# Kernel optimization log

Hardware: AMD Instinct MI355X
Metric: run time of the kernel (lower is better)

The kernel has to match this reference:

```python
import jax, jax.numpy as jnp
import numpy as np

K1, K2, K3 = 6, 4, 3  # knn_graph k (loop=True -> self included, dist 0 is always top)


def _sqdist(a, b):
    # a: [B,N,3], b: [B,M,3] -> [B,N,M] squared euclidean distances
    an = jnp.sum(a * a, -1)[:, :, None]
    bn = jnp.sum(b * b, -1)[:, None, :]
    return an + bn - 2.0 * jnp.einsum('bnd,bmd->bnm', a, b)


def _knn_idx(pos, k):
    # for each point, indices of its k nearest neighbors (self included, loop=True)
    d = _sqdist(pos, pos)                 # [B,N,N]
    _, idx = jax.lax.top_k(-d, k)         # [B,N,k]
    return idx


def _gather(a, idx):
    # a: [B,N,...], idx: [B,...] -> per-cloud gather
    return jax.vmap(lambda ab, ib: ab[ib])(a, idx)


def _fps(pos, m):
    # farthest point sampling on one cloud [N,3], deterministic start at index 0
    min_d = jnp.sum((pos - pos[0]) ** 2, -1)  # [N]

    def step(min_d, _):
        idx = jnp.argmax(min_d)
        d = jnp.sum((pos - pos[idx]) ** 2, -1)
        return jnp.minimum(min_d, d), idx

    _, idxs = jax.lax.scan(step, min_d, None, length=m - 1)
    return jnp.concatenate([jnp.zeros((1,), dtype=idxs.dtype), idxs])


def _pn_layer(h, pos, k, W1, b1, W2, b2):
    # PointNetLayer: gather h_i/h_j/pos_i/pos_j over knn edges, MLP, max-aggregate
    idx = _knn_idx(pos, k)                       # [B,N,k]
    h_j = _gather(h, idx)                        # [B,N,k,C]
    pos_j = _gather(pos, idx)                    # [B,N,k,3]
    rel = pos_j - pos[:, :, None, :]             # pos_j - pos_i
    h_i = jnp.broadcast_to(h[:, :, None, :], h_j.shape)
    inp = jnp.concatenate([h_i, h_j, rel], -1)   # [B,N,k,2C+3]
    msg = jnp.maximum(inp @ W1 + b1, 0.0) @ W2 + b2
    return jnp.max(msg, axis=2)                  # scatter-max == dense max over k


def _forward(x, pos, W11, b11, W12, b12, W21, b21, W22, b22, W31, b31, W32, b32, Wr, br):
    h = jax.nn.relu(_pn_layer(x, pos, K1, W11, b11, W12, b12))
    idx = jax.vmap(lambda p: _fps(p, p.shape[0] // 2))(pos)   # ratio=0.5
    pos, h = _gather(pos, idx), _gather(h, idx)
    h = jax.nn.relu(_pn_layer(h, pos, K2, W21, b21, W22, b22))
    idx = jax.vmap(lambda p: _fps(p, p.shape[0] // 2))(pos)
    pos, h = _gather(pos, idx), _gather(h, idx)
    h = jax.nn.relu(_pn_layer(h, pos, K3, W31, b31, W32, b32))
    g = jnp.max(h, axis=1)                        # global_max_pool
    return g @ Wr + br                            # [B,10]


def _lin(key, fin, fout):
    k1, k2 = jax.random.split(key)
    lim = 1.0 / np.sqrt(fin)
    W = jax.random.uniform(k1, (fin, fout), minval=-lim, maxval=lim, dtype=jnp.float32)
    b = jax.random.uniform(k2, (fout,), minval=-lim, maxval=lim, dtype=jnp.float32)
    return W, b


def setup_inputs() -> dict:
    key = jax.random.key(0)
    ks = jax.random.split(key, 10)
    B, N = 16, 4096
    x = jax.random.normal(ks[0], (B, N, 1), dtype=jnp.float32)
    pos = jax.random.uniform(ks[1], (B, N, 3), dtype=jnp.float32)
    W11, b11 = _lin(ks[2], 1 * 2 + 3, 32)
    W12, b12 = _lin(ks[3], 32, 32)
    W21, b21 = _lin(ks[4], 32 * 2 + 3, 32)
    W22, b22 = _lin(ks[5], 32, 32)
    W31, b31 = _lin(ks[6], 32 * 2 + 3, 32)
    W32, b32 = _lin(ks[7], 32, 32)
    Wr, br = _lin(ks[8], 32, 10)
    return dict(x=x, pos=pos, W11=W11, b11=b11, W12=W12, b12=b12,
                W21=W21, b21=b21, W22=W22, b22=b22,
                W31=W31, b31=b31, W32=W32, b32=b32, Wr=Wr, br=br)


def reference(x, pos, W11, b11, W12, b12, W21, b21, W22, b22, W31, b31, W32, b32, Wr, br):
    return _forward(x, pos, W11, b11, W12, b12, W21, b21, W22, b22,
                    W31, b31, W32, b32, Wr, br)
```

## Files before the change

kernel.cpp:

```cpp
#include <hip/hip_runtime.h>

#define BATCH 16
#define NP1 4096
#define NP2 2048
#define NP3 1024

typedef float v2f __attribute__((ext_vector_type(2)));

__device__ __forceinline__ float f_add(float a, float b) { return __fadd_rn(a, b); }
__device__ __forceinline__ float f_mul(float a, float b) { return __fmul_rn(a, b); }
__device__ __forceinline__ float f_sub(float a, float b) { return __fsub_rn(a, b); }
__device__ __forceinline__ float sqnorm3(float x, float y, float z) {
  return f_add(f_add(f_mul(x, x), f_mul(y, y)), f_mul(z, z));
}

__device__ __forceinline__ unsigned long long u64max(unsigned long long a,
                                                     unsigned long long b) {
  return a > b ? a : b;
}
__device__ __forceinline__ unsigned long long u64min(unsigned long long a,
                                                     unsigned long long b) {
  return a < b ? a : b;
}
__device__ __forceinline__ double dmax(double a, double b) { return __builtin_fmax(a, b); }

template<int CTRL, int RMASK>
__device__ __forceinline__ unsigned long long dpp_u64(unsigned long long k) {
  const int lo = __builtin_amdgcn_update_dpp(0, (int)(unsigned)k, CTRL, RMASK, 0xF, true);
  const int hi = __builtin_amdgcn_update_dpp(0, (int)(unsigned)(k >> 32), CTRL, RMASK, 0xF, true);
  return ((unsigned long long)(unsigned)hi << 32) | (unsigned)lo;
}
template<int CTRL, int RMASK>
__device__ __forceinline__ double dpp_dbl(double v) {
  return __longlong_as_double(
      (long long)dpp_u64<CTRL, RMASK>((unsigned long long)__double_as_longlong(v)));
}

#define KBIAS 0x00100000u

__device__ __forceinline__ double wave_max_keyd(double k) {
  k = dmax(k, dpp_dbl<0x111, 0xF>(k));
  k = dmax(k, dpp_dbl<0x112, 0xF>(k));
  k = dmax(k, dpp_dbl<0x114, 0xF>(k));
  k = dmax(k, dpp_dbl<0x118, 0xF>(k));
  k = dmax(k, dpp_dbl<0x142, 0xA>(k));
  k = dmax(k, dpp_dbl<0x143, 0xC>(k));
  return k;
}

template<int N, int M>
__device__ void fps_block(char* __restrict__ smem, const float* __restrict__ P,
                          int* __restrict__ samp, float* __restrict__ pos_out)
{
#pragma clang fp contract(off)
  constexpr int THREADS = 512;
  constexpr int E = N / THREADS;
  constexpr int P2 = E / 2;
  float4* pos4 = (float4*)smem;
  unsigned short* ord = (unsigned short*)(smem + 16 * N);
  int* sampL = (int*)(smem + 18 * N);
  unsigned* cursor = (unsigned*)(smem + 18 * N + 4 * M);
  double* kslots = (double*)(smem + 18 * N + 4 * M + 32);
  const int tid = threadIdx.x;
  const int lane = tid & 63, wv = tid >> 6;
  if (tid < 8) cursor[tid] = 0u;
  __syncthreads();
  int oct[E];
#pragma unroll
  for (int e = 0; e < E; ++e) {
    const int t = e * THREADS + tid;
    const float x = P[t * 3], y = P[t * 3 + 1], z = P[t * 3 + 2];
    pos4[t] = make_float4(x, y, z, 0.f);
    oct[e] = (x > 0.5f ? 1 : 0) | (y > 0.5f ? 2 : 0) | (z > 0.5f ? 4 : 0);
    atomicAdd(&cursor[oct[e]], 1u);
  }
  __syncthreads();
  if (tid == 0) {
    unsigned run = 0;
#pragma unroll
    for (int o = 0; o < 8; ++o) { const unsigned c = cursor[o]; cursor[o] = run; run += c; }
  }
  __syncthreads();
#pragma unroll
  for (int e = 0; e < E; ++e) {
    const unsigned d = atomicAdd(&cursor[oct[e]], 1u);
    ord[d] = (unsigned short)(e * THREADS + tid);
  }
  __syncthreads();
  const float4 p0 = pos4[0];
  const float x0 = p0.x, y0 = p0.y, z0 = p0.z;
  v2f X2[P2], Y2[P2], Z2[P2], MD2[P2];
  unsigned ILO[E];
  double key = 0.0;
  float mnx = 1e30f, mny = 1e30f, mnz = 1e30f;
  float mxx = -1e30f, mxy = -1e30f, mxz = -1e30f;
  {
    const v2f x0v = {x0, x0}, y0v = {y0, y0}, z0v = {z0, z0};
#pragma unroll
    for (int p = 0; p < P2; ++p) {
      const int q0 = wv * (64 * E) + (2 * p) * 64 + lane;
      const int o0 = ord[q0], o1 = ord[q0 + 64];
      const float4 a0 = pos4[o0], a1 = pos4[o1];
      X2[p] = (v2f){a0.x, a1.x}; Y2[p] = (v2f){a0.y, a1.y}; Z2[p] = (v2f){a0.z, a1.z};
      mnx = fminf(mnx, fminf(a0.x, a1.x)); mxx = fmaxf(mxx, fmaxf(a0.x, a1.x));
      mny = fminf(mny, fminf(a0.y, a1.y)); mxy = fmaxf(mxy, fmaxf(a0.y, a1.y));
      mnz = fminf(mnz, fminf(a0.z, a1.z)); mxz = fmaxf(mxz, fmaxf(a0.z, a1.z));
      const v2f dx = X2[p] - x0v, dy = Y2[p] - y0v, dz = Z2[p] - z0v;
      MD2[p] = (dx * dx + dy * dy) + dz * dz;
      ILO[2 * p]     = 0xFFFFFFFFu - (unsigned)o0;
      ILO[2 * p + 1] = 0xFFFFFFFFu - (unsigned)o1;
      const unsigned long long k0 =
          ((unsigned long long)(__float_as_uint(MD2[p].x) + KBIAS) << 32) | ILO[2 * p];
      const unsigned long long k1 =
          ((unsigned long long)(__float_as_uint(MD2[p].y) + KBIAS) << 32) | ILO[2 * p + 1];
      key = dmax(key, dmax(__longlong_as_double((long long)k0),
                           __longlong_as_double((long long)k1)));
    }
  }
#pragma unroll
  for (int off = 1; off < 64; off <<= 1) {
    mnx = fminf(mnx, __shfl_xor(mnx, off)); mxx = fmaxf(mxx, __shfl_xor(mxx, off));
    mny = fminf(mny, __shfl_xor(mny, off)); mxy = fmaxf(mxy, __shfl_xor(mxy, off));
    mnz = fminf(mnz, __shfl_xor(mnz, off)); mxz = fmaxf(mxz, __shfl_xor(mxz, off));
  }
  if (tid == 0) sampL[0] = 0;
  bool dirty = true;
  double wkey = 0.0;
#pragma unroll 1
  for (int s = 1; s < M; ++s) {
    if (dirty) wkey = wave_max_keyd(key);
    const int pb = s & 1;
    if (lane == 63) kslots[pb * 8 + wv] = wkey;
    __syncthreads();
    double v0 = kslots[pb * 8 + 0], v1 = kslots[pb * 8 + 1];
    double v2 = kslots[pb * 8 + 2], v3 = kslots[pb * 8 + 3];
    double v4 = kslots[pb * 8 + 4], v5 = kslots[pb * 8 + 5];
    double v6 = kslots[pb * 8 + 6], v7 = kslots[pb * 8 + 7];
    v0 = dmax(v0, v1); v2 = dmax(v2, v3); v4 = dmax(v4, v5); v6 = dmax(v6, v7);
    v0 = dmax(v0, v2); v4 = dmax(v4, v6);
    v0 = dmax(v0, v4);
    const unsigned long long kb = (unsigned long long)__double_as_longlong(v0);
    const int gi = (int)(0xFFFFFFFFu - (unsigned)kb);
    const float4 sp = pos4[gi];
    if (tid == 0) sampL[s] = gi;
    const float mdx = fmaxf(fmaxf(f_sub(mnx, sp.x), f_sub(sp.x, mxx)), 0.f);
    const float mdy = fmaxf(fmaxf(f_sub(mny, sp.y), f_sub(sp.y, mxy)), 0.f);
    const float mdz = fmaxf(fmaxf(f_sub(mnz, sp.z), f_sub(sp.z, mxz)), 0.f);
    const float mind2 = sqnorm3(mdx, mdy, mdz);
    const unsigned wmhi = (unsigned)__builtin_amdgcn_readlane(
        (int)(unsigned)((unsigned long long)__double_as_longlong(wkey) >> 32), 63) - KBIAS;
    const float wmaxf = __uint_as_float(wmhi);
    if (mind2 < wmaxf) {
      dirty = true;
      key = 0.0;
      const v2f sxv = {sp.x, sp.x}, syv = {sp.y, sp.y}, szv = {sp.z, sp.z};
#pragma unroll
      for (int p = 0; p < P2; ++p) {
        const v2f dx = X2[p] - sxv, dy = Y2[p] - syv, dz = Z2[p] - szv;
        const v2f d = (dx * dx + dy * dy) + dz * dz;
        MD2[p] = __builtin_elementwise_min(MD2[p], d);
        const unsigned long long k0 =
            ((unsigned long long)(__float_as_uint(MD2[p].x) + KBIAS) << 32) | ILO[2 * p];
        const unsigned long long k1 =
            ((unsigned long long)(__float_as_uint(MD2[p].y) + KBIAS) << 32) | ILO[2 * p + 1];
        key = dmax(key, dmax(__longlong_as_double((long long)k0),
                             __longlong_as_double((long long)k1)));
      }
    } else {
      dirty = false;
    }
  }
  __syncthreads();
  for (int s2 = tid; s2 < M; s2 += THREADS) {
    const int g = sampL[s2];
    samp[s2] = g;
    const float4 sp2 = pos4[g];
    pos_out[3 * s2 + 0] = sp2.x;
    pos_out[3 * s2 + 1] = sp2.y;
    pos_out[3 * s2 + 2] = sp2.z;
  }
}

__device__ __forceinline__ float f4c(const float4& v, int c) {
  return c == 0 ? v.x : c == 1 ? v.y : c == 2 ? v.z : v.w;
}
__device__ __forceinline__ void fma4(float4& a, float v, const float4& w) {
  a.x += v * w.x; a.y += v * w.y; a.z += v * w.z; a.w += v * w.w;
}

template<int K, int C>
__device__ void pn_compute(
    const float4* __restrict__ sW1, const float4* __restrict__ sW2,
    const float* __restrict__ sb1, const float* __restrict__ sb2,
    const float* __restrict__ P, const float* __restrict__ Hsrc,
    const int* __restrict__ hmap, int i, float xi, float yi, float zi,
    const int* kn, float* __restrict__ outrow)
{
  float4 abase[8];
#pragma unroll
  for (int o = 0; o < 8; ++o)
    abase[o] = make_float4(sb1[4 * o], sb1[4 * o + 1], sb1[4 * o + 2], sb1[4 * o + 3]);
  if constexpr (C == 1) {
    const float v = Hsrc[hmap ? hmap[i] : i];
#pragma unroll
    for (int o = 0; o < 8; ++o) fma4(abase[o], v, sW1[o]);
  } else {
    const int ri = hmap ? hmap[i] : i;
    const float4* Hi = (const float4*)(Hsrc + (size_t)ri * C);
#pragma unroll
    for (int c4 = 0; c4 < C / 4; ++c4) {
      const float4 hv = Hi[c4];
#pragma unroll
      for (int q = 0; q < 4; ++q) {
        const float v = f4c(hv, q);
#pragma unroll
        for (int o = 0; o < 8; ++o) fma4(abase[o], v, sW1[(4 * c4 + q) * 8 + o]);
      }
    }
  }
  float4 best[8];
#pragma unroll
  for (int o = 0; o < 8; ++o)
    best[o] = make_float4(-__builtin_inff(), -__builtin_inff(), -__builtin_inff(), -__builtin_inff());

  auto edge_pair = [&](int j0, int j1) {
    float4 a0[8], a1[8];
#pragma unroll
    for (int o = 0; o < 8; ++o) { a0[o] = abase[o]; a1[o] = abase[o]; }
    const float rx0 = P[j0 * 3] - xi, ry0 = P[j0 * 3 + 1] - yi, rz0 = P[j0 * 3 + 2] - zi;
    const float rx1 = P[j1 * 3] - xi, ry1 = P[j1 * 3 + 1] - yi, rz1 = P[j1 * 3 + 2] - zi;
    if constexpr (C == 1) {
      const float v0 = Hsrc[hmap ? hmap[j0] : j0], v1 = Hsrc[hmap ? hmap[j1] : j1];
#pragma unroll
      for (int o = 0; o < 8; ++o) {
        const float4 w = sW1[C * 8 + o];
        fma4(a0[o], v0, w); fma4(a1[o], v1, w);
      }
    } else {
      const int r0i = hmap ? hmap[j0] : j0, r1i = hmap ? hmap[j1] : j1;
      const float4* Hj0 = (const float4*)(Hsrc + (size_t)r0i * C);
      const float4* Hj1 = (const float4*)(Hsrc + (size_t)r1i * C);
#pragma unroll
      for (int c4 = 0; c4 < C / 4; ++c4) {
        const float4 h0 = Hj0[c4], h1 = Hj1[c4];
#pragma unroll
        for (int q = 0; q < 4; ++q) {
          const float v0 = f4c(h0, q), v1 = f4c(h1, q);
#pragma unroll
          for (int o = 0; o < 8; ++o) {
            const float4 w = sW1[(C + 4 * c4 + q) * 8 + o];
            fma4(a0[o], v0, w); fma4(a1[o], v1, w);
          }
        }
      }
    }
    const float r0[3] = {rx0, ry0, rz0}, r1[3] = {rx1, ry1, rz1};
#pragma unroll
    for (int r = 0; r < 3; ++r) {
#pragma unroll
      for (int o = 0; o < 8; ++o) {
        const float4 w = sW1[(2 * C + r) * 8 + o];
        fma4(a0[o], r0[r], w); fma4(a1[o], r1[r], w);
      }
    }
#pragma unroll
    for (int o = 0; o < 8; ++o) {
      a0[o].x = fmaxf(a0[o].x, 0.f); a0[o].y = fmaxf(a0[o].y, 0.f);
      a0[o].z = fmaxf(a0[o].z, 0.f); a0[o].w = fmaxf(a0[o].w, 0.f);
      a1[o].x = fmaxf(a1[o].x, 0.f); a1[o].y = fmaxf(a1[o].y, 0.f);
      a1[o].z = fmaxf(a1[o].z, 0.f); a1[o].w = fmaxf(a1[o].w, 0.f);
    }
#pragma unroll
    for (int hf = 0; hf < 2; ++hf) {
      float4 m0[4], m1[4];
#pragma unroll
      for (int o4 = 0; o4 < 4; ++o4) {
        const int c0 = 16 * hf + 4 * o4;
        m0[o4] = make_float4(sb2[c0], sb2[c0 + 1], sb2[c0 + 2], sb2[c0 + 3]);
        m1[o4] = m0[o4];
      }
#pragma unroll
      for (int c = 0; c < 32; ++c) {
        const float v0 = f4c(a0[c >> 2], c & 3), v1 = f4c(a1[c >> 2], c & 3);
#pragma unroll
        for (int o4 = 0; o4 < 4; ++o4) {
          const float4 w = sW2[c * 8 + hf * 4 + o4];
          fma4(m0[o4], v0, w); fma4(m1[o4], v1, w);
        }
      }
#pragma unroll
      for (int o4 = 0; o4 < 4; ++o4) {
        float4& bb = best[hf * 4 + o4];
        bb.x = fmaxf(bb.x, fmaxf(m0[o4].x, m1[o4].x));
        bb.y = fmaxf(bb.y, fmaxf(m0[o4].y, m1[o4].y));
        bb.z = fmaxf(bb.z, fmaxf(m0[o4].z, m1[o4].z));
        bb.w = fmaxf(bb.w, fmaxf(m0[o4].w, m1[o4].w));
      }
    }
  };

#pragma unroll
  for (int e = 0; e + 1 < K; e += 2) edge_pair(kn[e], kn[e + 1]);

  float4* ho = (float4*)outrow;
#pragma unroll
  for (int o = 0; o < 8; ++o)
    ho[o] = make_float4(fmaxf(best[o].x, 0.0f), fmaxf(best[o].y, 0.0f),
                        fmaxf(best[o].z, 0.0f), fmaxf(best[o].w, 0.0f));
}

template<int K, int NC, int C, int THREADS>
__device__ void fused_knn_pn(char* __restrict__ smem,
    const float* __restrict__ P, const float* __restrict__ Hsrc,
    const int* __restrict__ hmap,
    const float* __restrict__ W1, const float* __restrict__ b1,
    const float* __restrict__ W2, const float* __restrict__ b2,
    float* __restrict__ hout, int s)
{
  constexpr int CIN = 2 * C + 3;
  float4* tile = (float4*)smem;
  float4* sW1 = (float4*)(smem + 16 * 1024);
  float4* sW2 = sW1 + CIN * 8;
  float* sb1 = (float*)(sW2 + 32 * 8);
  float* sb2 = sb1 + 32;
  const int tid = threadIdx.x;
  for (int t = tid; t < CIN * 8; t += THREADS) sW1[t] = ((const float4*)W1)[t];
  for (int t = tid; t < 32 * 8; t += THREADS) sW2[t] = ((const float4*)W2)[t];
  if (tid < 32) { sb1[tid] = b1[tid]; sb2[tid] = b2[tid]; }

  const float xi = P[s * 3], yi = P[s * 3 + 1], zi = P[s * 3 + 2];
  const float ni = sqnorm3(xi, yi, zi);
  float bd[K]; int bj[K];
#pragma unroll
  for (int t = 0; t < K; ++t) { bd[t] = __builtin_inff(); bj[t] = 0; }
  for (int base = 0; base < NC; base += 1024) {
    __syncthreads();
    for (int t = tid; t < 1024; t += THREADS) {
      const float* q = P + (size_t)(base + t) * 3;
      const float x = q[0], y = q[1], z = q[2];
      tile[t] = make_float4(x, y, z, sqnorm3(x, y, z));
    }
    __syncthreads();
#pragma unroll 2
    for (int t = 0; t < 1024; ++t) {
      const float4 q = tile[t];
      const float dot = f_add(f_add(f_mul(xi, q.x), f_mul(yi, q.y)), f_mul(zi, q.z));
      const float d = f_sub(f_add(ni, q.w), f_mul(2.0f, dot));
      if (d < bd[K - 1]) {
        bd[K - 1] = d; bj[K - 1] = base + t;
#pragma unroll
        for (int r = K - 1; r > 0; --r) {
          if (bd[r] < bd[r - 1]) {
            float td = bd[r]; bd[r] = bd[r - 1]; bd[r - 1] = td;
            int   tj = bj[r]; bj[r] = bj[r - 1]; bj[r - 1] = tj;
          } else break;
        }
      }
    }
  }
  pn_compute<K, C>(sW1, sW2, sb1, sb2, P, Hsrc, hmap, s, xi, yi, zi, bj,
                   hout + (size_t)s * 32);
}

template<int K, int NC>
__device__ void fused_knn_pn_quad(char* __restrict__ smem,
    const float* __restrict__ P, const float* __restrict__ Hsrc,
    const int* __restrict__ hmap,
    const float* __restrict__ W1, const float* __restrict__ b1,
    const float* __restrict__ W2, const float* __restrict__ b2,
    float* __restrict__ hout, int s, int q)
{
  constexpr int THREADS = 256;
  constexpr int RQ = NC / 4;
  constexpr int CIN = 67;
  float4* tile = (float4*)smem;
  float4* sW1 = (float4*)(smem + 16 * (NC + 4));
  float4* sW2 = sW1 + CIN * 8;
  float* sb1 = (float*)(sW2 + 32 * 8);
  float* sb2 = sb1 + 32;
  const int tid = threadIdx.x;

  for (int t = tid; t < NC; t += THREADS) {
    const float* c = P + (size_t)t * 3;
    const float x = c[0], y = c[1], z = c[2];
    tile[t + t / RQ] = make_float4(x, y, z, sqnorm3(x, y, z));
  }
  for (int t = tid; t < CIN * 8; t += THREADS) sW1[t] = ((const float4*)W1)[t];
  for (int t = tid; t < 32 * 8; t += THREADS) sW2[t] = ((const float4*)W2)[t];
  if (tid < 32) { sb1[tid] = b1[tid]; sb2[tid] = b2[tid]; }
  __syncthreads();

  const float4 qv = tile[s + s / RQ];
  const float xi = qv.x, yi = qv.y, zi = qv.z, ni = qv.w;
  float bd[4]; int bj[4];
#pragma unroll
  for (int t = 0; t < 4; ++t) { bd[t] = __builtin_inff(); bj[t] = 0; }
  const int sbase = q * (RQ + 1);
#pragma unroll 2
  for (int t = 0; t < RQ; ++t) {
    const float4 c = tile[sbase + t];
    const float dot = f_add(f_add(f_mul(xi, c.x), f_mul(yi, c.y)), f_mul(zi, c.z));
    const float d = f_sub(f_add(ni, c.w), f_mul(2.0f, dot));
    if (d < bd[3]) {
      bd[3] = d; bj[3] = q * RQ + t;
#pragma unroll
      for (int r = 3; r > 0; --r) {
        if (bd[r] < bd[r - 1]) {
          float td = bd[r]; bd[r] = bd[r - 1]; bd[r - 1] = td;
          int   tj = bj[r]; bj[r] = bj[r - 1]; bj[r - 1] = tj;
        } else break;
      }
    }
  }
  unsigned long long a0, a1, a2, a3;
  {
    auto mk = [](float d, int j) {
      unsigned u = __float_as_uint(d);
      u ^= (unsigned)((int)u >> 31) | 0x80000000u;
      return ((unsigned long long)u << 32) | (unsigned)j;
    };
    a0 = mk(bd[0], bj[0]); a1 = mk(bd[1], bj[1]);
    a2 = mk(bd[2], bj[2]); a3 = mk(bd[3], bj[3]);
  }
  {
    const unsigned long long b0 = __shfl_xor(a0, 1), b1_ = __shfl_xor(a1, 1),
                             b2_ = __shfl_xor(a2, 1), b3_ = __shfl_xor(a3, 1);
    const unsigned long long t0 = u64min(a0, b3_), t1 = u64min(a1, b2_),
                             t2 = u64min(a2, b1_), t3 = u64min(a3, b0);
    const unsigned long long u0 = u64min(t0, t2), u2 = u64max(t0, t2),
                             u1 = u64min(t1, t3), u3 = u64max(t1, t3);
    a0 = u64min(u0, u1); a1 = u64max(u0, u1);
    a2 = u64min(u2, u3); a3 = u64max(u2, u3);
  }
  {
    const unsigned long long b0 = __shfl_xor(a0, 2), b1_ = __shfl_xor(a1, 2),
                             b2_ = __shfl_xor(a2, 2), b3_ = __shfl_xor(a3, 2);
    const unsigned long long t0 = u64min(a0, b3_), t1 = u64min(a1, b2_),
                             t2 = u64min(a2, b1_), t3 = u64min(a3, b0);
    const unsigned long long u0 = u64min(t0, t2), u2 = u64max(t0, t2),
                             u1 = u64min(t1, t3), u3 = u64max(t1, t3);
    a0 = u64min(u0, u1); a1 = u64max(u0, u1);
    a2 = u64min(u2, u3); a3 = u64max(u2, u3);
  }
  const int e = (q < K) ? q : (K - 1);
  const unsigned long long ke = (e == 0) ? a0 : (e == 1) ? a1 : (e == 2) ? a2 : a3;
  const int jn = (int)(unsigned)ke;

  const int ri = hmap ? hmap[s] : s;
  const int rj = hmap ? hmap[jn] : jn;
  float4 acc[8];
#pragma unroll
  for (int o = 0; o < 8; ++o)
    acc[o] = make_float4(sb1[4 * o], sb1[4 * o + 1], sb1[4 * o + 2], sb1[4 * o + 3]);
  const float4* Hi = (const float4*)(Hsrc + (size_t)ri * 32);
#pragma unroll
  for (int c4 = 0; c4 < 8; ++c4) {
    const float4 hv = Hi[c4];
#pragma unroll
    for (int t = 0; t < 4; ++t) {
      const float v = f4c(hv, t);
#pragma unroll
      for (int o = 0; o < 8; ++o) fma4(acc[o], v, sW1[(4 * c4 + t) * 8 + o]);
    }
  }
  const float4* Hj = (const float4*)(Hsrc + (size_t)rj * 32);
#pragma unroll
  for (int c4 = 0; c4 < 8; ++c4) {
    const float4 hv = Hj[c4];
#pragma unroll
    for (int t = 0; t < 4; ++t) {
      const float v = f4c(hv, t);
#pragma unroll
      for (int o = 0; o < 8; ++o) fma4(acc[o], v, sW1[(32 + 4 * c4 + t) * 8 + o]);
    }
  }
  const float4 cj = tile[jn + jn / RQ];
  const float r3[3] = {cj.x - xi, cj.y - yi, cj.z - zi};
#pragma unroll
  for (int r = 0; r < 3; ++r)
#pragma unroll
    for (int o = 0; o < 8; ++o) fma4(acc[o], r3[r], sW1[(64 + r) * 8 + o]);
#pragma unroll
  for (int o = 0; o < 8; ++o) {
    acc[o].x = fmaxf(acc[o].x, 0.f); acc[o].y = fmaxf(acc[o].y, 0.f);
    acc[o].z = fmaxf(acc[o].z, 0.f); acc[o].w = fmaxf(acc[o].w, 0.f);
  }
  float4 m[8];
#pragma unroll
  for (int o = 0; o < 8; ++o)
    m[o] = make_float4(sb2[4 * o], sb2[4 * o + 1], sb2[4 * o + 2], sb2[4 * o + 3]);
#pragma unroll
  for (int c = 0; c < 32; ++c) {
    const float v = f4c(acc[c >> 2], c & 3);
#pragma unroll
    for (int o = 0; o < 8; ++o) fma4(m[o], v, sW2[c * 8 + o]);
  }
#pragma unroll
  for (int o = 0; o < 8; ++o) {
    float4 v = m[o];
    v.x = fmaxf(v.x, __shfl_xor(v.x, 1)); v.y = fmaxf(v.y, __shfl_xor(v.y, 1));
    v.z = fmaxf(v.z, __shfl_xor(v.z, 1)); v.w = fmaxf(v.w, __shfl_xor(v.w, 1));
    v.x = fmaxf(v.x, __shfl_xor(v.x, 2)); v.y = fmaxf(v.y, __shfl_xor(v.y, 2));
    v.z = fmaxf(v.z, __shfl_xor(v.z, 2)); v.w = fmaxf(v.w, __shfl_xor(v.w, 2));
    m[o] = v;
  }
  float4* ho = (float4*)(hout + (size_t)s * 32);
  {
    const float4 v0 = m[2 * q], v1 = m[2 * q + 1];
    ho[2 * q] = make_float4(fmaxf(v0.x, 0.f), fmaxf(v0.y, 0.f),
                            fmaxf(v0.z, 0.f), fmaxf(v0.w, 0.f));
    ho[2 * q + 1] = make_float4(fmaxf(v1.x, 0.f), fmaxf(v1.y, 0.f),
                                fmaxf(v1.z, 0.f), fmaxf(v1.w, 0.f));
  }
}

__global__ __launch_bounds__(512) void megaA(
    const float* __restrict__ x, const float* __restrict__ pos,
    const float* __restrict__ W11, const float* __restrict__ b11,
    const float* __restrict__ W12, const float* __restrict__ b12,
    int* __restrict__ samp1, float* __restrict__ pos2, float* __restrict__ h1full)
{
  __shared__ __align__(16) char smem[82112];
  if (blockIdx.x < BATCH) {
    const int b = blockIdx.x;
    fps_block<NP1, NP2>(smem, pos + (size_t)b * NP1 * 3, samp1 + b * NP2,
                        pos2 + (size_t)b * NP2 * 3);
  } else {
    const int id = blockIdx.x - BATCH;
    const int b = id >> 3;
    const int s = (id & 7) * 512 + threadIdx.x;
    fused_knn_pn<6, NP1, 1, 512>(smem, pos + (size_t)b * NP1 * 3, x + (size_t)b * NP1,
                                 nullptr, W11, b11, W12, b12,
                                 h1full + (size_t)b * NP1 * 32, s);
  }
}

__global__ __launch_bounds__(256) void megaB(
    const float* __restrict__ pos2, const int* __restrict__ samp1,
    const float* __restrict__ h1full,
    const float* __restrict__ W21, const float* __restrict__ b21,
    const float* __restrict__ W22, const float* __restrict__ b22,
    float* __restrict__ h2out)
{
  __shared__ __align__(16) char smem[(2048 + 4) * 16 + 67 * 8 * 16 + 32 * 8 * 16 + 256];
  const int b = blockIdx.x >> 4;
  const int s = ((blockIdx.x & 15) << 6) + (threadIdx.x >> 2);
  const int q = threadIdx.x & 3;
  fused_knn_pn_quad<4, NP2>(smem, pos2 + (size_t)b * NP2 * 3,
                            h1full + (size_t)b * NP1 * 32, samp1 + b * NP2,
                            W21, b21, W22, b22, h2out + (size_t)b * NP3 * 32, s, q);
}

__global__ __launch_bounds__(256) void megaC(
    const float* __restrict__ pos2, const float* __restrict__ h2out,
    const float* __restrict__ W31, const float* __restrict__ b31,
    const float* __restrict__ W32, const float* __restrict__ b32,
    float* __restrict__ h3full)
{
  __shared__ __align__(16) char smem[(1024 + 4) * 16 + 67 * 8 * 16 + 32 * 8 * 16 + 256];
  const int b = blockIdx.x >> 4;
  const int s = ((blockIdx.x & 15) << 6) + (threadIdx.x >> 2);
  const int q = threadIdx.x & 3;
  fused_knn_pn_quad<3, NP3>(smem, pos2 + (size_t)b * NP2 * 3,
                            h2out + (size_t)b * NP3 * 32, nullptr,
                            W31, b31, W32, b32, h3full + (size_t)b * NP3 * 32, s, q);
}

__global__ __launch_bounds__(256) void final_kernel(
    const float* __restrict__ h, const float* __restrict__ Wr,
    const float* __restrict__ br, float* __restrict__ out)
{
  __shared__ float red[8][32];
  __shared__ float g[32];
  const int b = blockIdx.x;
  const int c = threadIdx.x & 31, grp = threadIdx.x >> 5;
  const float* H = h + (size_t)b * NP3 * 32;
  float m = -__builtin_inff();
  for (int r = grp; r < NP3; r += 8) m = fmaxf(m, H[r * 32 + c]);
  red[grp][c] = m;
  __syncthreads();
  if (threadIdx.x < 32) {
    float v = red[0][c];
#pragma unroll
    for (int w = 1; w < 8; ++w) v = fmaxf(v, red[w][c]);
    g[c] = v;
  }
  __syncthreads();
  if (threadIdx.x < 10) {
    float v = br[threadIdx.x];
#pragma unroll
    for (int cc = 0; cc < 32; ++cc) v += g[cc] * Wr[cc * 10 + threadIdx.x];
    out[b * 10 + threadIdx.x] = v;
  }
}

extern "C" void kernel_launch(void* const* d_in, const int* in_sizes, int n_in,
                              void* d_out, int out_size, void* d_ws, size_t ws_size,
                              hipStream_t stream) {
  const float* x   = (const float*)d_in[0];
  const float* pos = (const float*)d_in[1];
  const float* W11 = (const float*)d_in[2];
  const float* b11 = (const float*)d_in[3];
  const float* W12 = (const float*)d_in[4];
  const float* b12 = (const float*)d_in[5];
  const float* W21 = (const float*)d_in[6];
  const float* b21 = (const float*)d_in[7];
  const float* W22 = (const float*)d_in[8];
  const float* b22 = (const float*)d_in[9];
  const float* W31 = (const float*)d_in[10];
  const float* b31 = (const float*)d_in[11];
  const float* W32 = (const float*)d_in[12];
  const float* b32 = (const float*)d_in[13];
  const float* Wr  = (const float*)d_in[14];
  const float* br  = (const float*)d_in[15];
  float* out = (float*)d_out;

  char* p = (char*)d_ws;
  auto alloc = [&](size_t bytes) {
    char* r = p; p += (bytes + 255) & ~(size_t)255; return r;
  };
  int*   samp1  = (int*)  alloc(sizeof(int)   * BATCH * NP2);
  float* pos2   = (float*)alloc(sizeof(float) * BATCH * NP2 * 3);
  float* h1full = (float*)alloc(sizeof(float) * BATCH * NP1 * 32);
  float* h2out  = (float*)alloc(sizeof(float) * BATCH * NP3 * 32);
  float* h3full = (float*)alloc(sizeof(float) * BATCH * NP3 * 32);

  megaA<<<BATCH + BATCH * (NP1 / 512), 512, 0, stream>>>(
      x, pos, W11, b11, W12, b12, samp1, pos2, h1full);
  megaB<<<BATCH * 16, 256, 0, stream>>>(
      pos2, samp1, h1full, W21, b21, W22, b22, h2out);
  megaC<<<BATCH * 16, 256, 0, stream>>>(
      pos2, h2out, W31, b31, W32, b32, h3full);
  final_kernel<<<BATCH, 256, 0, stream>>>(h3full, Wr, br, out);
}
```

Measured before the change: 1.491 ms.

## Streamline FPS reduction and batch KNN distance computation with early feature loads

The FPS kernel drops the key bias and splits the key max into two independent accumulators to shorten the dependency chain. The cross-wave reduction becomes one slot load per lane followed by a DPP max, replacing eight LDS reads per thread. The KNN scans compute eight distances before running the insertion sort, which exposes more ILP. The h_i feature loads are hoisted ahead of the neighbour search so their latency overlaps it. Removing KBIAS changes how zero distances encode into the key, and positive distances stay ordered, but the hoisted loads add register pressure.

Result: faster. 1.359 ms (-8.8%).

```diff
diff --git a/kernel.cpp b/kernel.cpp
--- a/kernel.cpp
+++ b/kernel.cpp
@@ -36,7 +36,6 @@
       (long long)dpp_u64<CTRL, RMASK>((unsigned long long)__double_as_longlong(v)));
 }
 
-#define KBIAS 0x00100000u
 
 __device__ __forceinline__ double wave_max_keyd(double k) {
   k = dmax(k, dpp_dbl<0x111, 0xF>(k));
@@ -63,6 +62,7 @@
   double* kslots = (double*)(smem + 18 * N + 4 * M + 32);
   const int tid = threadIdx.x;
   const int lane = tid & 63, wv = tid >> 6;
+  const int myslot = lane & 7;
   if (tid < 8) cursor[tid] = 0u;
   __syncthreads();
   int oct[E];
@@ -91,10 +91,11 @@
   const float x0 = p0.x, y0 = p0.y, z0 = p0.z;
   v2f X2[P2], Y2[P2], Z2[P2], MD2[P2];
   unsigned ILO[E];
-  double key = 0.0;
+  double key;
   float mnx = 1e30f, mny = 1e30f, mnz = 1e30f;
   float mxx = -1e30f, mxy = -1e30f, mxz = -1e30f;
   {
+    double ka = 0.0, kb = 0.0;
     const v2f x0v = {x0, x0}, y0v = {y0, y0}, z0v = {z0, z0};
 #pragma unroll
     for (int p = 0; p < P2; ++p) {
@@ -110,12 +111,14 @@
       ILO[2 * p]     = 0xFFFFFFFFu - (unsigned)o0;
       ILO[2 * p + 1] = 0xFFFFFFFFu - (unsigned)o1;
       const unsigned long long k0 =
-          ((unsigned long long)(__float_as_uint(MD2[p].x) + KBIAS) << 32) | ILO[2 * p];
+          ((unsigned long long)__float_as_uint(MD2[p].x) << 32) | ILO[2 * p];
       const unsigned long long k1 =
-          ((unsigned long long)(__float_as_uint(MD2[p].y) + KBIAS) << 32) | ILO[2 * p + 1];
-      key = dmax(key, dmax(__longlong_as_double((long long)k0),
-                           __longlong_as_double((long long)k1)));
-    }
+          ((unsigned long long)__float_as_uint(MD2[p].y) << 32) | ILO[2 * p + 1];
+      const double kp = dmax(__longlong_as_double((long long)k0),
+                             __longlong_as_double((long long)k1));
+      if (p & 1) kb = dmax(kb, kp); else ka = dmax(ka, kp);
+    }
+    key = dmax(ka, kb);
   }
 #pragma unroll
   for (int off = 1; off < 64; off <<= 1) {
@@ -132,14 +135,11 @@
     const int pb = s & 1;
     if (lane == 63) kslots[pb * 8 + wv] = wkey;
     __syncthreads();
-    double v0 = kslots[pb * 8 + 0], v1 = kslots[pb * 8 + 1];
-    double v2 = kslots[pb * 8 + 2], v3 = kslots[pb * 8 + 3];
-    double v4 = kslots[pb * 8 + 4], v5 = kslots[pb * 8 + 5];
-    double v6 = kslots[pb * 8 + 6], v7 = kslots[pb * 8 + 7];
-    v0 = dmax(v0, v1); v2 = dmax(v2, v3); v4 = dmax(v4, v5); v6 = dmax(v6, v7);
-    v0 = dmax(v0, v2); v4 = dmax(v4, v6);
-    v0 = dmax(v0, v4);
-    const unsigned long long kb = (unsigned long long)__double_as_longlong(v0);
+    double v = kslots[pb * 8 + myslot];
+    v = dmax(v, dpp_dbl<0xB1, 0xF>(v));
+    v = dmax(v, dpp_dbl<0x4E, 0xF>(v));
+    v = dmax(v, dpp_dbl<0x124, 0xF>(v));
+    const unsigned long long kb = (unsigned long long)__double_as_longlong(v);
     const int gi = (int)(0xFFFFFFFFu - (unsigned)kb);
     const float4 sp = pos4[gi];
     if (tid == 0) sampL[s] = gi;
@@ -148,11 +148,11 @@
     const float mdz = fmaxf(fmaxf(f_sub(mnz, sp.z), f_sub(sp.z, mxz)), 0.f);
     const float mind2 = sqnorm3(mdx, mdy, mdz);
     const unsigned wmhi = (unsigned)__builtin_amdgcn_readlane(
-        (int)(unsigned)((unsigned long long)__double_as_longlong(wkey) >> 32), 63) - KBIAS;
+        (int)(unsigned)((unsigned long long)__double_as_longlong(wkey) >> 32), 63);
     const float wmaxf = __uint_as_float(wmhi);
     if (mind2 < wmaxf) {
       dirty = true;
-      key = 0.0;
+      double ka = 0.0, kb2 = 0.0;
       const v2f sxv = {sp.x, sp.x}, syv = {sp.y, sp.y}, szv = {sp.z, sp.z};
 #pragma unroll
       for (int p = 0; p < P2; ++p) {
@@ -160,12 +160,14 @@
         const v2f d = (dx * dx + dy * dy) + dz * dz;
         MD2[p] = __builtin_elementwise_min(MD2[p], d);
         const unsigned long long k0 =
-            ((unsigned long long)(__float_as_uint(MD2[p].x) + KBIAS) << 32) | ILO[2 * p];
+            ((unsigned long long)__float_as_uint(MD2[p].x) << 32) | ILO[2 * p];
         const unsigned long long k1 =
-            ((unsigned long long)(__float_as_uint(MD2[p].y) + KBIAS) << 32) | ILO[2 * p + 1];
-        key = dmax(key, dmax(__longlong_as_double((long long)k0),
-                             __longlong_as_double((long long)k1)));
-      }
+            ((unsigned long long)__float_as_uint(MD2[p].y) << 32) | ILO[2 * p + 1];
+        const double kp = dmax(__longlong_as_double((long long)k0),
+                               __longlong_as_double((long long)k1));
+        if (p & 1) kb2 = dmax(kb2, kp); else ka = dmax(ka, kp);
+      }
+      key = dmax(ka, kb2);
     } else {
       dirty = false;
     }
@@ -341,19 +343,26 @@
       tile[t] = make_float4(x, y, z, sqnorm3(x, y, z));
     }
     __syncthreads();
-#pragma unroll 2
-    for (int t = 0; t < 1024; ++t) {
-      const float4 q = tile[t];
-      const float dot = f_add(f_add(f_mul(xi, q.x), f_mul(yi, q.y)), f_mul(zi, q.z));
-      const float d = f_sub(f_add(ni, q.w), f_mul(2.0f, dot));
-      if (d < bd[K - 1]) {
-        bd[K - 1] = d; bj[K - 1] = base + t;
-#pragma unroll
-        for (int r = K - 1; r > 0; --r) {
-          if (bd[r] < bd[r - 1]) {
-            float td = bd[r]; bd[r] = bd[r - 1]; bd[r - 1] = td;
-            int   tj = bj[r]; bj[r] = bj[r - 1]; bj[r - 1] = tj;
-          } else break;
+#pragma unroll 1
+    for (int t = 0; t < 1024; t += 8) {
+      float dv[8];
+#pragma unroll
+      for (int u = 0; u < 8; ++u) {
+        const float4 q = tile[t + u];
+        const float dot = f_add(f_add(f_mul(xi, q.x), f_mul(yi, q.y)), f_mul(zi, q.z));
+        dv[u] = f_sub(f_add(ni, q.w), f_mul(2.0f, dot));
+      }
+#pragma unroll
+      for (int u = 0; u < 8; ++u) {
+        if (dv[u] < bd[K - 1]) {
+          bd[K - 1] = dv[u]; bj[K - 1] = base + t + u;
+#pragma unroll
+          for (int r = K - 1; r > 0; --r) {
+            if (bd[r] < bd[r - 1]) {
+              float td = bd[r]; bd[r] = bd[r - 1]; bd[r - 1] = td;
+              int   tj = bj[r]; bj[r] = bj[r - 1]; bj[r - 1] = tj;
+            } else break;
+          }
         }
       }
     }
@@ -392,23 +401,39 @@
 
   const float4 qv = tile[s + s / RQ];
   const float xi = qv.x, yi = qv.y, zi = qv.z, ni = qv.w;
+
+  const int ri = hmap ? hmap[s] : s;
+  float4 hi4[8];
+  {
+    const float4* Hi = (const float4*)(Hsrc + (size_t)ri * 32);
+#pragma unroll
+    for (int c4 = 0; c4 < 8; ++c4) hi4[c4] = Hi[c4];
+  }
+
   float bd[4]; int bj[4];
 #pragma unroll
   for (int t = 0; t < 4; ++t) { bd[t] = __builtin_inff(); bj[t] = 0; }
   const int sbase = q * (RQ + 1);
-#pragma unroll 2
-  for (int t = 0; t < RQ; ++t) {
-    const float4 c = tile[sbase + t];
-    const float dot = f_add(f_add(f_mul(xi, c.x), f_mul(yi, c.y)), f_mul(zi, c.z));
-    const float d = f_sub(f_add(ni, c.w), f_mul(2.0f, dot));
-    if (d < bd[3]) {
-      bd[3] = d; bj[3] = q * RQ + t;
-#pragma unroll
-      for (int r = 3; r > 0; --r) {
-        if (bd[r] < bd[r - 1]) {
-          float td = bd[r]; bd[r] = bd[r - 1]; bd[r - 1] = td;
-          int   tj = bj[r]; bj[r] = bj[r - 1]; bj[r - 1] = tj;
-        } else break;
+#pragma unroll 1
+  for (int t = 0; t < RQ; t += 8) {
+    float dv[8];
+#pragma unroll
+    for (int u = 0; u < 8; ++u) {
+      const float4 c = tile[sbase + t + u];
+      const float dot = f_add(f_add(f_mul(xi, c.x), f_mul(yi, c.y)), f_mul(zi, c.z));
+      dv[u] = f_sub(f_add(ni, c.w), f_mul(2.0f, dot));
+    }
+#pragma unroll
+    for (int u = 0; u < 8; ++u) {
+      if (dv[u] < bd[3]) {
+        bd[3] = dv[u]; bj[3] = q * RQ + t + u;
+#pragma unroll
+        for (int r = 3; r > 0; --r) {
+          if (bd[r] < bd[r - 1]) {
+            float td = bd[r]; bd[r] = bd[r - 1]; bd[r - 1] = td;
+            int   tj = bj[r]; bj[r] = bj[r - 1]; bj[r - 1] = tj;
+          } else break;
+        }
       }
     }
   }
@@ -446,16 +471,20 @@
   const unsigned long long ke = (e == 0) ? a0 : (e == 1) ? a1 : (e == 2) ? a2 : a3;
   const int jn = (int)(unsigned)ke;
 
-  const int ri = hmap ? hmap[s] : s;
   const int rj = hmap ? hmap[jn] : jn;
+  float4 hj4[8];
+  {
+    const float4* Hj = (const float4*)(Hsrc + (size_t)rj * 32);
+#pragma unroll
+    for (int c4 = 0; c4 < 8; ++c4) hj4[c4] = Hj[c4];
+  }
   float4 acc[8];
 #pragma unroll
   for (int o = 0; o < 8; ++o)
     acc[o] = make_float4(sb1[4 * o], sb1[4 * o + 1], sb1[4 * o + 2], sb1[4 * o + 3]);
-  const float4* Hi = (const float4*)(Hsrc + (size_t)ri * 32);
 #pragma unroll
   for (int c4 = 0; c4 < 8; ++c4) {
-    const float4 hv = Hi[c4];
+    const float4 hv = hi4[c4];
 #pragma unroll
     for (int t = 0; t < 4; ++t) {
       const float v = f4c(hv, t);
@@ -463,10 +492,9 @@
       for (int o = 0; o < 8; ++o) fma4(acc[o], v, sW1[(4 * c4 + t) * 8 + o]);
     }
   }
-  const float4* Hj = (const float4*)(Hsrc + (size_t)rj * 32);
 #pragma unroll
   for (int c4 = 0; c4 < 8; ++c4) {
-    const float4 hv = Hj[c4];
+    const float4 hv = hj4[c4];
 #pragma unroll
     for (int t = 0; t < 4; ++t) {
       const float v = f4c(hv, t);
```
